# Kernel optimization log

Measured on AMD Instinct MI355X. Metric: run time of the kernel, lower is better.

The kernel has to match this reference:

```python
import jax, jax.numpy as jnp
import numpy as np

# ---- dims ----
N_NODES = 33      # nodes per graph (33-bus grid)
SEQ     = 24      # time steps per sample
BATCH   = 64      # samples
G       = BATCH * SEQ          # total graphs in the batch
EPG     = 64                   # directed edges per graph
E       = G * EPG              # total edges
N       = G * N_NODES          # total nodes
IN_CH   = 2
HID     = 64
HEADS   = 8
HC      = HID * HEADS          # 512
EDGE_DIM = 3
LSTM1_H = 128
LSTM2_H = 64
N_CLASSES = 4
NEG_SLOPE = 0.2


def setup_inputs() -> dict:
    key = jax.random.key(0)
    ks = jax.random.split(key, 32)
    rng = np.random.default_rng(0)

    # block-structured edge_index: every edge stays inside its own graph
    off = np.repeat(np.arange(G, dtype=np.int64) * N_NODES, EPG)
    src = rng.integers(0, N_NODES, E) + off
    dst = rng.integers(0, N_NODES, E) + off
    edge_index = jnp.asarray(np.stack([src, dst]), dtype=jnp.int32)

    def glorot(k, shape):
        fan = shape[0] + shape[-1]
        s = jnp.sqrt(6.0 / fan).astype(jnp.float32)
        return jax.random.uniform(k, shape, jnp.float32, -s, s)

    inp = dict(
        x=jax.random.normal(ks[0], (N, IN_CH), jnp.float32),
        edge_index=edge_index,
        edge_attr=jax.random.uniform(ks[1], (E, EDGE_DIM), jnp.float32),
        # GATv2 layer 1 (concat=True)
        g1_Wl=glorot(ks[2], (IN_CH, HC)),
        g1_Wr=glorot(ks[3], (IN_CH, HC)),
        g1_We=glorot(ks[4], (EDGE_DIM, HC)),
        g1_att=glorot(ks[5], (HEADS, HID)),
        g1_b=jnp.zeros((HC,), jnp.float32),
        # GATv2 layer 2 (concat=False -> head mean)
        g2_Wl=glorot(ks[6], (HC, HC)),
        g2_Wr=glorot(ks[7], (HC, HC)),
        g2_We=glorot(ks[8], (EDGE_DIM, HC)),
        g2_att=glorot(ks[9], (HEADS, HID)),
        g2_b=jnp.zeros((HID,), jnp.float32),
        # LSTM1: input 33*64=2112 -> 128, gates ordered (i,f,g,o)
        l1_Wih=0.05 * jax.random.normal(ks[10], (4 * LSTM1_H, N_NODES * HID), jnp.float32),
        l1_Whh=0.05 * jax.random.normal(ks[11], (4 * LSTM1_H, LSTM1_H), jnp.float32),
        l1_bih=jnp.zeros((4 * LSTM1_H,), jnp.float32),
        l1_bhh=jnp.zeros((4 * LSTM1_H,), jnp.float32),
        # LSTM2: 128 -> 64
        l2_Wih=0.05 * jax.random.normal(ks[12], (4 * LSTM2_H, LSTM1_H), jnp.float32),
        l2_Whh=0.05 * jax.random.normal(ks[13], (4 * LSTM2_H, LSTM2_H), jnp.float32),
        l2_bih=jnp.zeros((4 * LSTM2_H,), jnp.float32),
        l2_bhh=jnp.zeros((4 * LSTM2_H,), jnp.float32),
        # FC 64 -> n_classes
        fc_W=0.05 * jax.random.normal(ks[14], (N_CLASSES, LSTM2_H), jnp.float32),
        fc_b=jnp.zeros((N_CLASSES,), jnp.float32),
    )
    return inp


def _gatv2(x, edge_attr, src, dst, Wl, Wr, We, att, b, concat):
    """PyG GATv2Conv with edge_dim, add_self_loops semantics omitted is NOT used:
    we follow the message math: m = leaky_relu(xl[src]+xr[dst]+We@e),
    alpha = segment_softmax(<m,att>, dst), out = scatter_add(alpha * xl[src])."""
    n = x.shape[0]
    xl = (x @ Wl).reshape(n, HEADS, HID)      # [N,H,C]
    xr = (x @ Wr).reshape(n, HEADS, HID)
    em = (edge_attr @ We).reshape(-1, HEADS, HID)  # [E,H,C]
    m = jax.nn.leaky_relu(xl[src] + xr[dst] + em, NEG_SLOPE)
    logits = jnp.einsum('ehc,hc->eh', m, att)          # [E,H]
    mx = jax.ops.segment_max(logits, dst, num_segments=n)   # [N,H]
    ex = jnp.exp(logits - mx[dst])
    den = jax.ops.segment_sum(ex, dst, num_segments=n)
    alpha = ex / (den[dst] + 1e-16)                    # [E,H]
    out = jax.ops.segment_sum(xl[src] * alpha[:, :, None], dst, num_segments=n)  # [N,H,C]
    out = out.reshape(n, HC) if concat else out.mean(axis=1)
    return out + b


def _lstm(x, Wih, Whh, bih, bhh, hsz):
    B = x.shape[0]
    h0 = jnp.zeros((B, hsz), x.dtype)
    c0 = jnp.zeros((B, hsz), x.dtype)

    def step(carry, xt):
        h, c = carry
        gates = xt @ Wih.T + h @ Whh.T + bih + bhh
        i, f, g, o = jnp.split(gates, 4, axis=-1)
        i = jax.nn.sigmoid(i); f = jax.nn.sigmoid(f)
        g = jnp.tanh(g);       o = jax.nn.sigmoid(o)
        c = f * c + i * g
        h = o * jnp.tanh(c)
        return (h, c), h

    _, ys = jax.lax.scan(step, (h0, c0), x.transpose(1, 0, 2))  # [T,B,H]
    return ys.transpose(1, 0, 2)


def reference(x, edge_index, edge_attr,
              g1_Wl, g1_Wr, g1_We, g1_att, g1_b,
              g2_Wl, g2_Wr, g2_We, g2_att, g2_b,
              l1_Wih, l1_Whh, l1_bih, l1_bhh,
              l2_Wih, l2_Whh, l2_bih, l2_bhh,
              fc_W, fc_b):
    src, dst = edge_index[0], edge_index[1]
    h = jax.nn.elu(_gatv2(x, edge_attr, src, dst, g1_Wl, g1_Wr, g1_We, g1_att, g1_b, True))
    h = jax.nn.elu(_gatv2(h, edge_attr, src, dst, g2_Wl, g2_Wr, g2_We, g2_att, g2_b, False))
    seq = h.reshape(BATCH, SEQ, N_NODES * HID)          # [B,T,2112]
    seq = _lstm(seq, l1_Wih, l1_Whh, l1_bih, l1_bhh, LSTM1_H)
    seq = _lstm(seq, l2_Wih, l2_Whh, l2_bih, l2_bhh, LSTM2_H)
    last = seq[:, -1, :]                                 # [B,64]
    return last @ fc_W.T + fc_b                          # [B,n_classes]
```

## Files before the change

### kernel.cpp

```cpp
#include <hip/hip_runtime.h>
#include <math.h>

#define N_NODES 33
#define SEQ 24
#define BATCH 64
#define G_GRAPHS (BATCH * SEQ)
#define EPG 64
#define E_EDGES (G_GRAPHS * EPG)
#define N_TOTAL (G_GRAPHS * N_NODES)
#define HID 64
#define HEADS 8
#define HC (HID * HEADS)
#define LSTM1_H 128
#define LSTM2_H 64
#define NEG_SLOPE 0.2f
#define CONV_BLOCKS (128 + 264)

__device__ __forceinline__ float sigmoidf_(float x) { return 1.f / (1.f + expf(-x)); }
__device__ __forceinline__ float eluf_(float x) { return x > 0.f ? x : expm1f(x); }
__device__ __forceinline__ float lreluf_(float x) { return x > 0.f ? x : NEG_SLOPE * x; }

typedef __attribute__((ext_vector_type(4))) float f32x4;
typedef _Float16 half_t;
typedef __attribute__((ext_vector_type(8))) _Float16 halfx8;

__device__ __forceinline__ void gl2lds16(const void* g, void* l) {
  __builtin_amdgcn_global_load_lds(
      (__attribute__((address_space(1))) const unsigned int*)g,
      (__attribute__((address_space(3))) unsigned int*)l, 16, 0, 0);
}

__global__ __launch_bounds__(512) void gat1_kernel(
    const float* __restrict__ x, const int* __restrict__ src, const int* __restrict__ dst,
    const float* __restrict__ ea, const float* __restrict__ Wl, const float* __restrict__ Wr,
    const float* __restrict__ We, const float* __restrict__ att, const float* __restrict__ bias,
    half_t* __restrict__ h1, int g0, int gat_blocks,
    const float* __restrict__ g2Wl, const float* __restrict__ g2Wr,
    half_t* __restrict__ B2, const float* __restrict__ W1, half_t* __restrict__ W1f) {
  const int tid = threadIdx.x;

  __shared__ alignas(16) float Wl_s[2 * 512];
  __shared__ alignas(16) float Wr_s[2 * 512];
  __shared__ alignas(16) float We_s[3 * 512];
  __shared__ alignas(16) float att_s[512];
  __shared__ float xs0_s[N_NODES + 1], xs1_s[N_NODES + 1];
  __shared__ float easX[EPG], easY[EPG], easZ[EPG];
  __shared__ float logit_s[HEADS * 65];
  __shared__ int sloc[EPG], dloc[EPG], deg[N_NODES], start[N_NODES], fill[N_NODES], elist[EPG];
  __shared__ float tr[64 * 65];

  if ((int)blockIdx.x >= gat_blocks) {
    int cb = blockIdx.x - gat_blocks;
    if (cb < 128) {
      int kt = cb & 7, nt = cb >> 3;
      int k0 = kt * 64, n0 = nt * 64;
      int r = tid >> 6, c = tid & 63;
      #pragma unroll
      for (int rr = 0; rr < 8; ++rr) {
        int kl = rr * 8 + r;
        int n = n0 + c;
        float v = (n < 512) ? g2Wl[(size_t)(k0 + kl) * 512 + n]
                            : g2Wr[(size_t)(k0 + kl) * 512 + n - 512];
        tr[kl * 65 + c] = v;
      }
      __syncthreads();
      #pragma unroll
      for (int rr = 0; rr < 8; ++rr) {
        int nl = rr * 8 + r;
        B2[(size_t)(n0 + nl) * 512 + k0 + c] = (half_t)tr[c * 65 + nl];
      }
    } else {
      int base = (cb - 128) * 4096 + tid;
      #pragma unroll
      for (int i = 0; i < 8; ++i) {
        int idx = base + i * 512;
        if (idx < 512 * 2112) W1f[idx] = (half_t)W1[idx];
      }
    }
    return;
  }

  const int g = g0 + blockIdx.x;
  const int nb = g * N_NODES, eb = g * EPG;
  const int lb = blockIdx.x * N_NODES;

  for (int i = tid; i < 1024; i += 512) { Wl_s[i] = Wl[i]; Wr_s[i] = Wr[i]; }
  for (int i = tid; i < 1536; i += 512) We_s[i] = We[i];
  if (tid < 512) att_s[tid] = att[tid];
  if (tid < 2 * N_NODES) {
    float v = x[nb * 2 + tid];
    if (tid & 1) xs1_s[tid >> 1] = v; else xs0_s[tid >> 1] = v;
  }
  if (tid < EPG) {
    easX[tid] = ea[(eb + tid) * 3 + 0];
    easY[tid] = ea[(eb + tid) * 3 + 1];
    easZ[tid] = ea[(eb + tid) * 3 + 2];
    sloc[tid] = src[eb + tid] - nb;
    dloc[tid] = dst[eb + tid] - nb;
  }
  if (tid < N_NODES) { deg[tid] = 0; fill[tid] = 0; }
  __syncthreads();
  if (tid < EPG) atomicAdd(&deg[dloc[tid]], 1);
  __syncthreads();
  if (tid == 0) { int a = 0; for (int n = 0; n < N_NODES; ++n) { start[n] = a; a += deg[n]; } }
  __syncthreads();
  if (tid < EPG) { int d = dloc[tid]; int p = atomicAdd(&fill[d], 1); elist[start[d] + p] = tid; }

  {
    int h = tid >> 6, e = tid & 63;
    int s = sloc[e], d = dloc[e];
    float xs0 = xs0_s[s], xs1 = xs1_s[s], xd0 = xs0_s[d], xd1 = xs1_s[d];
    float e0 = easX[e], e1 = easY[e], e2 = easZ[e];
    float acc = 0.f;
    int base = h * 64;
    #pragma unroll
    for (int c4 = 0; c4 < 16; ++c4) {
      int j = base + c4 * 4;
      f32x4 wl0 = *(const f32x4*)(Wl_s + j);
      f32x4 wl1 = *(const f32x4*)(Wl_s + 512 + j);
      f32x4 wr0 = *(const f32x4*)(Wr_s + j);
      f32x4 wr1 = *(const f32x4*)(Wr_s + 512 + j);
      f32x4 we0 = *(const f32x4*)(We_s + j);
      f32x4 we1 = *(const f32x4*)(We_s + 512 + j);
      f32x4 we2 = *(const f32x4*)(We_s + 1024 + j);
      f32x4 at  = *(const f32x4*)(att_s + j);
      #pragma unroll
      for (int q = 0; q < 4; ++q) {
        float v = xs0 * wl0[q] + xs1 * wl1[q]
                + xd0 * wr0[q] + xd1 * wr1[q]
                + e0 * we0[q] + e1 * we1[q] + e2 * we2[q];
        acc += lreluf_(v) * at[q];
      }
    }
    logit_s[h * 65 + e] = acc;
  }
  __syncthreads();

  {
    int h = tid >> 6, n = tid & 63;
    if (n < N_NODES) {
      int s0 = start[n], dn = deg[n];
      float mx = -1e30f;
      for (int i = 0; i < dn; ++i) mx = fmaxf(mx, logit_s[h * 65 + elist[s0 + i]]);
      float den = 0.f;
      for (int i = 0; i < dn; ++i) den += expf(logit_s[h * 65 + elist[s0 + i]] - mx);
      float inv = 1.f / (den + 1e-16f);
      for (int i = 0; i < dn; ++i) {
        int e = elist[s0 + i];
        logit_s[h * 65 + e] = expf(logit_s[h * 65 + e] - mx) * inv;
      }
    }
  }
  __syncthreads();

  for (int t = tid; t < N_NODES * 64; t += 512) {
    int n = t >> 6, jb = t & 63;
    int j0 = jb * 8, h = jb >> 3;
    f32x4 wa0 = *(const f32x4*)(Wl_s + j0);
    f32x4 wa1 = *(const f32x4*)(Wl_s + j0 + 4);
    f32x4 wb0 = *(const f32x4*)(Wl_s + 512 + j0);
    f32x4 wb1 = *(const f32x4*)(Wl_s + 512 + j0 + 4);
    float acc[8] = {};
    int s0 = start[n], dn = deg[n];
    for (int i = 0; i < dn; ++i) {
      int e = elist[s0 + i]; int s = sloc[e];
      float a = logit_s[h * 65 + e];
      float ax0 = a * xs0_s[s], ax1 = a * xs1_s[s];
      #pragma unroll
      for (int q = 0; q < 4; ++q) {
        acc[q]     += ax0 * wa0[q] + ax1 * wb0[q];
        acc[4 + q] += ax0 * wa1[q] + ax1 * wb1[q];
      }
    }
    f32x4 b0 = *(const f32x4*)(bias + j0);
    f32x4 b1 = *(const f32x4*)(bias + j0 + 4);
    halfx8 vh;
    #pragma unroll
    for (int cc = 0; cc < 8; ++cc) {
      float bb = (cc < 4) ? b0[cc] : b1[cc - 4];
      vh[cc] = (half_t)eluf_(acc[cc] + bb);
    }
    *(halfx8*)(h1 + (size_t)(lb + n) * HC + j0) = vh;
  }
}

#define LDA8(S, rr, c) \
  (*(const halfx8*)((S) + (rr) * 64 + ((((c) ^ ((rr) & 7))) << 3)))

__global__ __launch_bounds__(256, 4) void gemm_m97(
    const half_t* __restrict__ A, const half_t* __restrict__ B,
    half_t* __restrict__ C, int M) {
  __shared__ alignas(16) half_t lds[128 * 132];

  half_t* const As = lds;
  half_t* const Bs = lds + 8192;

  const int R = M >> 7;
  const int nwg = R * 8;
  const int cpx = nwg >> 3;
  const int bid = blockIdx.x;
  const int swz = (bid & 7) * cpx + (bid >> 3);
  const int ct = swz & 7, r = swz >> 3;

  const int tid = threadIdx.x;
  const int wave = tid >> 6, lane = tid & 63;
  const int wm = wave >> 1, wn = wave & 1;
  const int bm = r << 7, bn = ct << 7;

  const int rl = lane >> 3;
  const int gc = ((lane & 7) ^ rl) << 3;
  const int fr = lane & 15;
  const int kq = lane >> 4;

  f32x4 acc[4][4];
  #pragma unroll
  for (int tm = 0; tm < 4; ++tm)
    #pragma unroll
    for (int tn = 0; tn < 4; ++tn) acc[tm][tn] = {0.f, 0.f, 0.f, 0.f};

  for (int t = 0; t < 8; ++t) {
    #pragma unroll
    for (int i = 0; i < 4; ++i) {
      int r0 = i * 32 + wave * 8;
      gl2lds16(A + (size_t)(bm + r0 + rl) * 512 + t * 64 + gc, As + r0 * 64);
    }
    #pragma unroll
    for (int i = 0; i < 4; ++i) {
      int r0 = i * 32 + wave * 8;
      gl2lds16(B + (size_t)(bn + r0 + rl) * 512 + t * 64 + gc, Bs + r0 * 64);
    }
    __syncthreads();

    #pragma unroll
    for (int ks = 0; ks < 2; ++ks) {
      halfx8 af[4], bf[4];
      #pragma unroll
      for (int tm = 0; tm < 4; ++tm)
        af[tm] = LDA8(As, wm * 64 + tm * 16 + fr, ks * 4 + kq);
      #pragma unroll
      for (int tn = 0; tn < 4; ++tn)
        bf[tn] = LDA8(Bs, wn * 64 + tn * 16 + fr, ks * 4 + kq);
      #pragma unroll
      for (int tm = 0; tm < 4; ++tm)
        #pragma unroll
        for (int tn = 0; tn < 4; ++tn)
          acc[tm][tn] = __builtin_amdgcn_mfma_f32_16x16x32_f16(
              af[tm], bf[tn], acc[tm][tn], 0, 0, 0);
    }
    __syncthreads();
  }

  half_t* Cs = lds;
  const int rq4 = (lane >> 4) * 4;
  const int cl0 = lane & 15;
  #pragma unroll
  for (int tm = 0; tm < 4; ++tm)
    #pragma unroll
    for (int tn = 0; tn < 4; ++tn) {
      int cl = wn * 64 + tn * 16 + cl0;
      #pragma unroll
      for (int rr = 0; rr < 4; ++rr)
        Cs[(wm * 64 + tm * 16 + rq4 + rr) * 132 + cl] = (half_t)acc[tm][tn][rr];
    }
  __syncthreads();
  #pragma unroll
  for (int pass = 0; pass < 8; ++pass) {
    int row = pass * 16 + (tid >> 4);
    int col = (tid & 15) * 8;
    halfx8 v = *(const halfx8*)(Cs + row * 132 + col);
    *(halfx8*)(C + (size_t)(bm + row) * 1024 + bn + col) = v;
  }
}

__global__ __launch_bounds__(256) void gemm_f16_splitk(
    const half_t* __restrict__ A, const half_t* __restrict__ B,
    float* __restrict__ Cp, const float* __restrict__ bias1, const float* __restrict__ bias2,
    int M, int N) {
  constexpr int SA = 2112;
  __shared__ half_t lds[(64 + 64) * 64];
  half_t* A_s = lds;
  half_t* B_s = A_s + 2 * 64 * 32;

  const int part = blockIdx.y;
  const int koff = part ? 576 + (part - 1) * 512 : 0;
  const int kend = part ? 512 : 576;
  const half_t* Ap = A + koff;
  const half_t* Bp = B + koff;
  float* C = Cp + (size_t)part * M * N;

  const int R = M / 64, NT = N / 64;
  int b = blockIdx.x;
  int xcd = b & 7, q = b >> 3;
  int ct = q % NT, rg = q / NT;
  int r = rg * 8 + xcd;
  if (r >= R) return;

  const int tid = threadIdx.x;
  const int wave = tid >> 6, lane = tid & 63;
  const int wm = wave >> 1, wn = wave & 1;
  const int bm = r * 64, bn = ct * 64;

  const int rA = lane >> 2;
  const int swz = (rA & 3) ^ ((rA >> 2) & 3);
  const int cA = ((lane & 3) ^ swz) * 8;

  f32x4 acc[2][2];
  #pragma unroll
  for (int tm = 0; tm < 2; ++tm)
    #pragma unroll
    for (int tn = 0; tn < 2; ++tn) acc[tm][tn] = {0.f, 0.f, 0.f, 0.f};

  for (int k0 = 0; k0 < kend; k0 += 64) {
    #pragma unroll
    for (int p = 0; p < 2; ++p) {
      int kk = k0 + p * 32;
      int row = wave * 16;
      gl2lds16(Ap + (size_t)(bm + row + rA) * SA + kk + cA,
               A_s + p * 64 * 32 + row * 32);
      gl2lds16(Bp + (size_t)(bn + row + rA) * SA + kk + cA,
               B_s + p * 64 * 32 + row * 32);
    }
    __syncthreads();
    const int fr = lane & 15;
    const int fs = (fr & 3) ^ ((fr >> 2) & 3);
    const int fk = ((lane >> 4) ^ fs) * 8;
    #pragma unroll
    for (int p = 0; p < 2; ++p) {
      const int pA = p * 64 * 32, pB = p * 64 * 32;
      halfx8 af[2], bf[2];
      #pragma unroll
      for (int tm = 0; tm < 2; ++tm) {
        int rr = (wm * 2 + tm) * 16 + fr;
        af[tm] = *(const halfx8*)(A_s + pA + rr * 32 + fk);
      }
      #pragma unroll
      for (int tn = 0; tn < 2; ++tn) {
        int rr = (wn * 2 + tn) * 16 + fr;
        bf[tn] = *(const halfx8*)(B_s + pB + rr * 32 + fk);
      }
      #pragma unroll
      for (int tm = 0; tm < 2; ++tm)
        #pragma unroll
        for (int tn = 0; tn < 2; ++tn)
          acc[tm][tn] = __builtin_amdgcn_mfma_f32_16x16x32_f16(af[tm], bf[tn], acc[tm][tn], 0, 0, 0);
    }
    __syncthreads();
  }

  const int col0 = lane & 15, rq = (lane >> 4) * 4;
  #pragma unroll
  for (int tm = 0; tm < 2; ++tm)
    #pragma unroll
    for (int tn = 0; tn < 2; ++tn) {
      int col = bn + (wn * 2 + tn) * 16 + col0;
      float badd = (part == 0) ? (bias1[col] + bias2[col]) : 0.f;
      #pragma unroll
      for (int rr = 0; rr < 4; ++rr) {
        int row = bm + (wm * 2 + tm) * 16 + rq + rr;
        C[(size_t)row * N + col] = acc[tm][tn][rr] + badd;
      }
    }
}

__global__ __launch_bounds__(512) void gat2_kernel(
    const half_t* __restrict__ xlr, const int* __restrict__ src, const int* __restrict__ dst,
    const float* __restrict__ ea, const float* __restrict__ We,
    const float* __restrict__ att, const float* __restrict__ bias,
    half_t* __restrict__ h2, int g0) {
  __shared__ alignas(16) float We_s[3 * 512];
  __shared__ alignas(16) float att_s[512];
  __shared__ float b_s[HID];
  __shared__ float easX[EPG], easY[EPG], easZ[EPG];
  __shared__ float logit_s[HEADS * 65];
  __shared__ int sloc[EPG], dloc[EPG], deg[N_NODES], start[N_NODES], fill[N_NODES], elist[EPG];

  const int g = g0 + blockIdx.x, tid = threadIdx.x;
  const int nb = g * N_NODES, eb = g * EPG;
  const int lb = blockIdx.x * N_NODES;
  const int wave = tid >> 6, lane = tid & 63;

  for (int i = tid; i < 1536; i += 512) We_s[i] = We[i];
  if (tid < 512) att_s[tid] = att[tid];
  if (tid < HID) b_s[tid] = bias[tid];
  if (tid < EPG) {
    easX[tid] = ea[(eb + tid) * 3 + 0];
    easY[tid] = ea[(eb + tid) * 3 + 1];
    easZ[tid] = ea[(eb + tid) * 3 + 2];
    sloc[tid] = src[eb + tid] - nb;
    dloc[tid] = dst[eb + tid] - nb;
  }
  if (tid < N_NODES) { deg[tid] = 0; fill[tid] = 0; }
  __syncthreads();
  if (tid < EPG) atomicAdd(&deg[dloc[tid]], 1);
  __syncthreads();
  if (tid == 0) { int a = 0; for (int n = 0; n < N_NODES; ++n) { start[n] = a; a += deg[n]; } }
  __syncthreads();
  if (tid < EPG) { int d = dloc[tid]; int p = atomicAdd(&fill[d], 1); elist[start[d] + p] = tid; }
  __syncthreads();

  const int j0 = lane * 8;
  float w0[8], w1[8], w2[8], at8[8];
  #pragma unroll
  for (int q = 0; q < 8; ++q) {
    w0[q] = We_s[j0 + q];
    w1[q] = We_s[512 + j0 + q];
    w2[q] = We_s[1024 + j0 + q];
    at8[q] = att_s[j0 + q];
  }

  for (int e = wave; e < EPG; e += 8) {
    int s = sloc[e], d = dloc[e];
    halfx8 xlv = *((const halfx8*)(xlr + (size_t)(lb + s) * 1024) + lane);
    halfx8 xrv = *((const halfx8*)(xlr + (size_t)(lb + d) * 1024 + 512) + lane);
    float e0 = easX[e], e1 = easY[e], e2 = easZ[e];
    float acc = 0.f;
    #pragma unroll
    for (int q = 0; q < 8; ++q) {
      float v = (float)xlv[q] + (float)xrv[q] + e0 * w0[q] + e1 * w1[q] + e2 * w2[q];
      acc += lreluf_(v) * at8[q];
    }
    acc += __shfl_xor(acc, 1, 64);
    acc += __shfl_xor(acc, 2, 64);
    acc += __shfl_xor(acc, 4, 64);
    if ((lane & 7) == 0) logit_s[(lane >> 3) * 65 + e] = acc;
  }
  __syncthreads();

  {
    int h = tid >> 6, n = tid & 63;
    if (n < N_NODES) {
      int s0 = start[n], dn = deg[n];
      float mx = -1e30f;
      for (int i = 0; i < dn; ++i) mx = fmaxf(mx, logit_s[h * 65 + elist[s0 + i]]);
      float den = 0.f;
      for (int i = 0; i < dn; ++i) den += expf(logit_s[h * 65 + elist[s0 + i]] - mx);
      float inv = 1.f / (den + 1e-16f);
      for (int i = 0; i < dn; ++i) {
        int e = elist[s0 + i];
        logit_s[h * 65 + e] = expf(logit_s[h * 65 + e] - mx) * inv;
      }
    }
  }
  __syncthreads();

  for (int n = wave; n < N_NODES; n += 8) {
    float acc = 0.f;
    int s0 = start[n], dn = deg[n];
    for (int i = 0; i < dn; ++i) {
      int e = elist[s0 + i], s = sloc[e];
      const half_t* row = xlr + (size_t)(lb + s) * 1024 + lane;
      #pragma unroll
      for (int h = 0; h < 8; ++h)
        acc += logit_s[h * 65 + e] * (float)row[h * 64];
    }
    float v = eluf_(acc * 0.125f + b_s[lane]);
    h2[(size_t)(nb + n) * HID + lane] = (half_t)v;
  }
}

__global__ __launch_bounds__(1024, 4) void lstm_all(
    const float* __restrict__ X0, const float* __restrict__ X1,
    const float* __restrict__ X2p, const float* __restrict__ X3,
    const float* __restrict__ Whh1,
    const float* __restrict__ Wih2, const float* __restrict__ bih2,
    const float* __restrict__ bhh2, const float* __restrict__ Whh2,
    const float* __restrict__ fcW, const float* __restrict__ fcb,
    float* __restrict__ out) {
  __shared__ float hs1[LSTM1_H], cs1[LSTM1_H], p1[512], gs1[512];
  __shared__ float Y1s[SEQ][LSTM1_H];
  __shared__ float hs2[LSTM2_H], cs2[LSTM2_H], p2[4 * 256], gs2[256];
  const int tid = threadIdx.x, b = blockIdx.x;
  const int j = tid & 511, half = tid >> 9;

  float4 w1[16];
  {
    const float4* wp = (const float4*)(Whh1 + (size_t)j * LSTM1_H + half * 64);
    #pragma unroll
    for (int q = 0; q < 16; ++q) w1[q] = wp[q];
  }
  if (tid < LSTM1_H) { hs1[tid] = 0.f; cs1[tid] = 0.f; }
  __syncthreads();
  for (int t = 0; t < SEQ; ++t) {
    const float* hb = hs1 + half * 64;
    float acc = 0.f;
    #pragma unroll
    for (int q = 0; q < 16; ++q) {
      acc += w1[q].x * hb[4 * q] + w1[q].y * hb[4 * q + 1]
           + w1[q].z * hb[4 * q + 2] + w1[q].w * hb[4 * q + 3];
    }
    if (half) p1[j] = acc;
    __syncthreads();
    if (!half) {
      size_t xo = ((size_t)b * SEQ + t) * 512 + j;
      gs1[j] = acc + p1[j] + X0[xo] + X1[xo] + X2p[xo] + X3[xo];
    }
    __syncthreads();
    if (tid < LSTM1_H) {
      float ig = sigmoidf_(gs1[tid]);
      float fg = sigmoidf_(gs1[LSTM1_H + tid]);
      float gg = tanhf(gs1[2 * LSTM1_H + tid]);
      float og = sigmoidf_(gs1[3 * LSTM1_H + tid]);
      float c = fg * cs1[tid] + ig * gg;
      cs1[tid] = c;
      float h = og * tanhf(c);
      hs1[tid] = h;
      Y1s[t][tid] = h;
    }
    __syncthreads();
  }

  const int j2 = tid & 255, qt = tid >> 8;
  float4 w2x[8], w2h[4];
  {
    const float4* wxp = (const float4*)(Wih2 + (size_t)j2 * LSTM1_H + qt * 32);
    #pragma unroll
    for (int q = 0; q < 8; ++q) w2x[q] = wxp[q];
    const float4* whp = (const float4*)(Whh2 + (size_t)j2 * LSTM2_H + qt * 16);
    #pragma unroll
    for (int q = 0; q < 4; ++q) w2h[q] = whp[q];
  }
  if (tid < LSTM2_H) { hs2[tid] = 0.f; cs2[tid] = 0.f; }
  __syncthreads();
  for (int t = 0; t < SEQ; ++t) {
    const float* y = Y1s[t] + qt * 32;
    const float* hb = hs2 + qt * 16;
    float acc = 0.f;
    #pragma unroll
    for (int q = 0; q < 8; ++q) {
      acc += w2x[q].x * y[4 * q] + w2x[q].y * y[4 * q + 1]
           + w2x[q].z * y[4 * q + 2] + w2x[q].w * y[4 * q + 3];
    }
    #pragma unroll
    for (int q = 0; q < 4; ++q) {
      acc += w2h[q].x * hb[4 * q] + w2h[q].y * hb[4 * q + 1]
           + w2h[q].z * hb[4 * q + 2] + w2h[q].w * hb[4 * q + 3];
    }
    p2[qt * 256 + j2] = acc;
    __syncthreads();
    if (qt == 0)
      gs2[j2] = p2[j2] + p2[256 + j2] + p2[512 + j2] + p2[768 + j2]
              + bih2[j2] + bhh2[j2];
    __syncthreads();
    if (tid < LSTM2_H) {
      float ig = sigmoidf_(gs2[tid]);
      float fg = sigmoidf_(gs2[LSTM2_H + tid]);
      float gg = tanhf(gs2[2 * LSTM2_H + tid]);
      float og = sigmoidf_(gs2[3 * LSTM2_H + tid]);
      float c = fg * cs2[tid] + ig * gg;
      cs2[tid] = c;
      hs2[tid] = og * tanhf(c);
    }
    __syncthreads();
  }
  if (tid < 4) {
    float acc = fcb[tid];
    #pragma unroll
    for (int k = 0; k < LSTM2_H; ++k) acc += fcW[tid * LSTM2_H + k] * hs2[k];
    out[b * 4 + tid] = acc;
  }
}

extern "C" void kernel_launch(void* const* d_in, const int* in_sizes, int n_in,
                              void* d_out, int out_size, void* d_ws, size_t ws_size,
                              hipStream_t stream) {
  const float* x       = (const float*)d_in[0];
  const int*   eidx    = (const int*)d_in[1];
  const float* eattr   = (const float*)d_in[2];
  const float* g1_Wl   = (const float*)d_in[3];
  const float* g1_Wr   = (const float*)d_in[4];
  const float* g1_We   = (const float*)d_in[5];
  const float* g1_att  = (const float*)d_in[6];
  const float* g1_b    = (const float*)d_in[7];
  const float* g2_Wl   = (const float*)d_in[8];
  const float* g2_Wr   = (const float*)d_in[9];
  const float* g2_We   = (const float*)d_in[10];
  const float* g2_att  = (const float*)d_in[11];
  const float* g2_b    = (const float*)d_in[12];
  const float* l1_Wih  = (const float*)d_in[13];
  const float* l1_Whh  = (const float*)d_in[14];
  const float* l1_bih  = (const float*)d_in[15];
  const float* l1_bhh  = (const float*)d_in[16];
  const float* l2_Wih  = (const float*)d_in[17];
  const float* l2_Whh  = (const float*)d_in[18];
  const float* l2_bih  = (const float*)d_in[19];
  const float* l2_bhh  = (const float*)d_in[20];
  const float* fc_W    = (const float*)d_in[21];
  const float* fc_b    = (const float*)d_in[22];
  float* out = (float*)d_out;

  const int* src = eidx;
  const int* dst = eidx + E_EDGES;

  const int cand[4] = {1, 2, 3, 6};
  int nchunks = 0;
  half_t *h1 = nullptr, *xlr2c = nullptr, *h2 = nullptr, *B2 = nullptr, *W1f = nullptr;
  float *X1p = nullptr;
  int chunk_g = 0, chunk_n = 0;
  for (int ci = 0; ci < 4; ++ci) {
    int C = cand[ci];
    int CG = G_GRAPHS / C, CN = CG * N_NODES;
    char* p = (char*)d_ws;
    auto alloc = [&](size_t bytes) { char* r = p; p += (bytes + 255) & ~(size_t)255; return r; };
    half_t* t_h1    = (half_t*)alloc((size_t)CN * HC * 2);
    half_t* t_xlr2c = (half_t*)alloc((size_t)CN * 1024 * 2);
    half_t* t_h2    = (half_t*)alloc((size_t)G_GRAPHS * 2112 * 2);
    half_t* t_B2    = (half_t*)alloc((size_t)1024 * 512 * 2);
    half_t* t_W1f   = (half_t*)alloc((size_t)512 * 2112 * 2);
    float*  t_X1p   = (float*)alloc((size_t)4 * G_GRAPHS * 512 * 4);
    if ((size_t)(p - (char*)d_ws) <= ws_size) {
      nchunks = C; chunk_g = CG; chunk_n = CN;
      h1 = t_h1; xlr2c = t_xlr2c; h2 = t_h2; B2 = t_B2; W1f = t_W1f;
      X1p = t_X1p;
      break;
    }
  }
  if (nchunks == 0) return;

  for (int c = 0; c < nchunks; ++c) {
    int g0 = c * chunk_g;
    int extra = (c == 0) ? CONV_BLOCKS : 0;
    gat1_kernel<<<chunk_g + extra, 512, 0, stream>>>(
        x, src, dst, eattr, g1_Wl, g1_Wr, g1_We, g1_att, g1_b, h1, g0, chunk_g,
        g2_Wl, g2_Wr, B2, l1_Wih, W1f);
    int gblocks = (chunk_n / 128) * 8;
    gemm_m97<<<gblocks, 256, 0, stream>>>(h1, B2, xlr2c, chunk_n);
    gat2_kernel<<<chunk_g, 512, 0, stream>>>(xlr2c, src, dst, eattr, g2_We,
                                             g2_att, g2_b, h2, g0);
  }

  {
    dim3 grid(192, 4);
    gemm_f16_splitk<<<grid, 256, 0, stream>>>(h2, W1f, X1p, l1_bih, l1_bhh,
                                              G_GRAPHS, 512);
  }

  {
    size_t PS = (size_t)G_GRAPHS * 512;
    lstm_all<<<BATCH, 1024, 0, stream>>>(X1p, X1p + PS, X1p + 2 * PS, X1p + 3 * PS,
                                         l1_Whh, l2_Wih, l2_bih, l2_bhh, l2_Whh,
                                         fc_W, fc_b, out);
  }
}
```

Before: 340.9 us.

## Halve LSTM block size, one thread per gate row, prefetch input projections

The LSTM kernel now runs with 512 threads per block. Each thread holds a full recurrent weight row in registers, so the partial-sum exchange through shared memory and one barrier per timestep go away in both LSTM layers. The precomputed input-projection terms for the next timestep are prefetched into registers to hide global-memory latency, and the LSTM2 bias is hoisted out of the loop. In exchange, register pressure rises (w2x and w2h need up to 192 floats) and only half the threads work in the second layer, so spills or lower occupancy are possible.

```diff
diff --git a/kernel.cpp b/kernel.cpp
--- a/kernel.cpp
+++ b/kernel.cpp
@@ -458,7 +458,7 @@
   }
 }
 
-__global__ __launch_bounds__(1024, 4) void lstm_all(
+__global__ __launch_bounds__(512) void lstm_all(
     const float* __restrict__ X0, const float* __restrict__ X1,
     const float* __restrict__ X2p, const float* __restrict__ X3,
     const float* __restrict__ Whh1,
@@ -466,34 +466,42 @@
     const float* __restrict__ bhh2, const float* __restrict__ Whh2,
     const float* __restrict__ fcW, const float* __restrict__ fcb,
     float* __restrict__ out) {
-  __shared__ float hs1[LSTM1_H], cs1[LSTM1_H], p1[512], gs1[512];
+  __shared__ float hs1[LSTM1_H], cs1[LSTM1_H], gs1[512];
   __shared__ float Y1s[SEQ][LSTM1_H];
-  __shared__ float hs2[LSTM2_H], cs2[LSTM2_H], p2[4 * 256], gs2[256];
+  __shared__ float hs2[LSTM2_H], cs2[LSTM2_H], gs2[256];
   const int tid = threadIdx.x, b = blockIdx.x;
-  const int j = tid & 511, half = tid >> 9;
-
-  float4 w1[16];
+
+  float4 w1[32];
   {
-    const float4* wp = (const float4*)(Whh1 + (size_t)j * LSTM1_H + half * 64);
-    #pragma unroll
-    for (int q = 0; q < 16; ++q) w1[q] = wp[q];
+    const float4* wp = (const float4*)(Whh1 + (size_t)tid * LSTM1_H);
+    #pragma unroll
+    for (int q = 0; q < 32; ++q) w1[q] = wp[q];
   }
   if (tid < LSTM1_H) { hs1[tid] = 0.f; cs1[tid] = 0.f; }
-  __syncthreads();
+
+  const size_t xbase = (size_t)b * SEQ * 512 + tid;
+  float xn0 = X0[xbase], xn1 = X1[xbase], xn2 = X2p[xbase], xn3 = X3[xbase];
+  __syncthreads();
+
   for (int t = 0; t < SEQ; ++t) {
-    const float* hb = hs1 + half * 64;
-    float acc = 0.f;
-    #pragma unroll
-    for (int q = 0; q < 16; ++q) {
-      acc += w1[q].x * hb[4 * q] + w1[q].y * hb[4 * q + 1]
-           + w1[q].z * hb[4 * q + 2] + w1[q].w * hb[4 * q + 3];
-    }
-    if (half) p1[j] = acc;
-    __syncthreads();
-    if (!half) {
-      size_t xo = ((size_t)b * SEQ + t) * 512 + j;
-      gs1[j] = acc + p1[j] + X0[xo] + X1[xo] + X2p[xo] + X3[xo];
-    }
+    float a0 = 0.f, a1 = 0.f, a2 = 0.f, a3 = 0.f;
+    #pragma unroll
+    for (int q = 0; q < 8; ++q) {
+      const float4 h0 = *(const float4*)(hs1 + q * 16);
+      const float4 h1 = *(const float4*)(hs1 + q * 16 + 4);
+      const float4 h2 = *(const float4*)(hs1 + q * 16 + 8);
+      const float4 h3 = *(const float4*)(hs1 + q * 16 + 12);
+      a0 += w1[q*4+0].x * h0.x + w1[q*4+0].y * h0.y + w1[q*4+0].z * h0.z + w1[q*4+0].w * h0.w;
+      a1 += w1[q*4+1].x * h1.x + w1[q*4+1].y * h1.y + w1[q*4+1].z * h1.z + w1[q*4+1].w * h1.w;
+      a2 += w1[q*4+2].x * h2.x + w1[q*4+2].y * h2.y + w1[q*4+2].z * h2.z + w1[q*4+2].w * h2.w;
+      a3 += w1[q*4+3].x * h3.x + w1[q*4+3].y * h3.y + w1[q*4+3].z * h3.z + w1[q*4+3].w * h3.w;
+    }
+    float g = (a0 + a1) + (a2 + a3) + ((xn0 + xn1) + (xn2 + xn3));
+    if (t + 1 < SEQ) {
+      size_t xo = xbase + (size_t)(t + 1) * 512;
+      xn0 = X0[xo]; xn1 = X1[xo]; xn2 = X2p[xo]; xn3 = X3[xo];
+    }
+    gs1[tid] = g;
     __syncthreads();
     if (tid < LSTM1_H) {
       float ig = sigmoidf_(gs1[tid]);
@@ -509,37 +517,48 @@
     __syncthreads();
   }
 
-  const int j2 = tid & 255, qt = tid >> 8;
-  float4 w2x[8], w2h[4];
-  {
-    const float4* wxp = (const float4*)(Wih2 + (size_t)j2 * LSTM1_H + qt * 32);
-    #pragma unroll
-    for (int q = 0; q < 8; ++q) w2x[q] = wxp[q];
-    const float4* whp = (const float4*)(Whh2 + (size_t)j2 * LSTM2_H + qt * 16);
-    #pragma unroll
-    for (int q = 0; q < 4; ++q) w2h[q] = whp[q];
+  float4 w2x[32], w2h[16];
+  float bb2 = 0.f;
+  if (tid < 256) {
+    const float4* wxp = (const float4*)(Wih2 + (size_t)tid * LSTM1_H);
+    #pragma unroll
+    for (int q = 0; q < 32; ++q) w2x[q] = wxp[q];
+    const float4* whp = (const float4*)(Whh2 + (size_t)tid * LSTM2_H);
+    #pragma unroll
+    for (int q = 0; q < 16; ++q) w2h[q] = whp[q];
+    bb2 = bih2[tid] + bhh2[tid];
   }
   if (tid < LSTM2_H) { hs2[tid] = 0.f; cs2[tid] = 0.f; }
   __syncthreads();
+
   for (int t = 0; t < SEQ; ++t) {
-    const float* y = Y1s[t] + qt * 32;
-    const float* hb = hs2 + qt * 16;
-    float acc = 0.f;
-    #pragma unroll
-    for (int q = 0; q < 8; ++q) {
-      acc += w2x[q].x * y[4 * q] + w2x[q].y * y[4 * q + 1]
-           + w2x[q].z * y[4 * q + 2] + w2x[q].w * y[4 * q + 3];
-    }
-    #pragma unroll
-    for (int q = 0; q < 4; ++q) {
-      acc += w2h[q].x * hb[4 * q] + w2h[q].y * hb[4 * q + 1]
-           + w2h[q].z * hb[4 * q + 2] + w2h[q].w * hb[4 * q + 3];
-    }
-    p2[qt * 256 + j2] = acc;
-    __syncthreads();
-    if (qt == 0)
-      gs2[j2] = p2[j2] + p2[256 + j2] + p2[512 + j2] + p2[768 + j2]
-              + bih2[j2] + bhh2[j2];
+    if (tid < 256) {
+      const float* y = Y1s[t];
+      float a0 = 0.f, a1 = 0.f, a2 = 0.f, a3 = 0.f;
+      #pragma unroll
+      for (int q = 0; q < 8; ++q) {
+        const float4 y0 = *(const float4*)(y + q * 16);
+        const float4 y1 = *(const float4*)(y + q * 16 + 4);
+        const float4 y2 = *(const float4*)(y + q * 16 + 8);
+        const float4 y3 = *(const float4*)(y + q * 16 + 12);
+        a0 += w2x[q*4+0].x * y0.x + w2x[q*4+0].y * y0.y + w2x[q*4+0].z * y0.z + w2x[q*4+0].w * y0.w;
+        a1 += w2x[q*4+1].x * y1.x + w2x[q*4+1].y * y1.y + w2x[q*4+1].z * y1.z + w2x[q*4+1].w * y1.w;
+        a2 += w2x[q*4+2].x * y2.x + w2x[q*4+2].y * y2.y + w2x[q*4+2].z * y2.z + w2x[q*4+2].w * y2.w;
+        a3 += w2x[q*4+3].x * y3.x + w2x[q*4+3].y * y3.y + w2x[q*4+3].z * y3.z + w2x[q*4+3].w * y3.w;
+      }
+      #pragma unroll
+      for (int q = 0; q < 4; ++q) {
+        const float4 h0 = *(const float4*)(hs2 + q * 16);
+        const float4 h1 = *(const float4*)(hs2 + q * 16 + 4);
+        const float4 h2 = *(const float4*)(hs2 + q * 16 + 8);
+        const float4 h3 = *(const float4*)(hs2 + q * 16 + 12);
+        a0 += w2h[q*4+0].x * h0.x + w2h[q*4+0].y * h0.y + w2h[q*4+0].z * h0.z + w2h[q*4+0].w * h0.w;
+        a1 += w2h[q*4+1].x * h1.x + w2h[q*4+1].y * h1.y + w2h[q*4+1].z * h1.z + w2h[q*4+1].w * h1.w;
+        a2 += w2h[q*4+2].x * h2.x + w2h[q*4+2].y * h2.y + w2h[q*4+2].z * h2.z + w2h[q*4+2].w * h2.w;
+        a3 += w2h[q*4+3].x * h3.x + w2h[q*4+3].y * h3.y + w2h[q*4+3].z * h3.z + w2h[q*4+3].w * h3.w;
+      }
+      gs2[tid] = (a0 + a1) + (a2 + a3) + bb2;
+    }
     __syncthreads();
     if (tid < LSTM2_H) {
       float ig = sigmoidf_(gs2[tid]);
@@ -552,6 +571,7 @@
     }
     __syncthreads();
   }
+
   if (tid < 4) {
     float acc = fcb[tid];
     #pragma unroll
@@ -636,8 +656,8 @@
 
   {
     size_t PS = (size_t)G_GRAPHS * 512;
-    lstm_all<<<BATCH, 1024, 0, stream>>>(X1p, X1p + PS, X1p + 2 * PS, X1p + 3 * PS,
-                                         l1_Whh, l2_Wih, l2_bih, l2_bhh, l2_Whh,
-                                         fc_W, fc_b, out);
+    lstm_all<<<BATCH, 512, 0, stream>>>(X1p, X1p + PS, X1p + 2 * PS, X1p + 3 * PS,
+                                        l1_Whh, l2_Wih, l2_bih, l2_bhh, l2_Whh,
+                                        fc_W, fc_b, out);
   }
 }
```

Result: no change. 345.2 us (+1.3%).
